# Kernel optimization log

Hardware: AMD Instinct MI355X
Metric: run time of the kernel (lower is better)

The kernel has to match this reference:

```python
import jax, jax.numpy as jnp
import numpy as np

B, S, L = 64, 512, 768


def setup_inputs() -> dict:
    key = jax.random.key(0)
    k1, k2 = jax.random.split(key)
    x = jax.random.normal(k1, (B, S, L), dtype=jnp.float32)
    # matches torch uniform_(-0.1, 0.1) init for the probe matrix b
    b = jax.random.uniform(k2, (L, L), minval=-0.1, maxval=0.1, dtype=jnp.float32)
    return {"x": x, "b": b}


def reference(x, b):
    # Original: z[b,i,j,h] = x_i - x_j; h = einsum('gh,bijh', b, z); dist = sum_g h^2
    # Identity: ||b @ (x_i - x_j)||^2 = ||p_i||^2 + ||p_j||^2 - 2 p_i . p_j,  p = x @ b^T
    p = jnp.einsum('gh,bsh->bsg', b, x)          # [B, S, L] projected points
    sq = jnp.sum(p * p, axis=-1)                 # [B, S]  squared norms
    gram = jnp.einsum('bsg,btg->bst', p, p)      # [B, S, S] inner products
    return sq[:, :, None] + sq[:, None, :] - 2.0 * gram  # [B, S, S]
```

## Files before the change

### kernel.cpp

```cpp
#include <hip/hip_runtime.h>
#include <hip/hip_bf16.h>


using bf16x8 = __attribute__((ext_vector_type(8))) __bf16;
using f32x4  = __attribute__((ext_vector_type(4))) float;
using fl4    = __attribute__((ext_vector_type(4))) float;
using u16x4  = __attribute__((ext_vector_type(4))) unsigned short;
using u32x4  = __attribute__((ext_vector_type(4))) unsigned int;

#define NB 64
#define NS 512
#define NL 768

__device__ __forceinline__ unsigned short f2bf(float f) {
  unsigned u = __builtin_bit_cast(unsigned, f);
  u += 0x7FFFu + ((u >> 16) & 1u);
  return (unsigned short)(u >> 16);
}

__device__ __forceinline__ void gload_lds16(const void* g, void* l) {
  __builtin_amdgcn_global_load_lds(
      (const __attribute__((address_space(1))) void*)g,
      (__attribute__((address_space(3))) void*)l, 16, 0, 0);
}

__device__ __forceinline__ bf16x8 cvt_bf8(fl4 a, fl4 b) {
  unsigned r0, r1, r2, r3;
  asm("v_cvt_pk_bf16_f32 %0, %1, %2" : "=v"(r0) : "v"(a[0]), "v"(a[1]));
  asm("v_cvt_pk_bf16_f32 %0, %1, %2" : "=v"(r1) : "v"(a[2]), "v"(a[3]));
  asm("v_cvt_pk_bf16_f32 %0, %1, %2" : "=v"(r2) : "v"(b[0]), "v"(b[1]));
  asm("v_cvt_pk_bf16_f32 %0, %1, %2" : "=v"(r3) : "v"(b[2]), "v"(b[3]));
  u32x4 t = {r0, r1, r2, r3};
  return __builtin_bit_cast(bf16x8, t);
}

__global__ __launch_bounds__(256) void k_cvt_b(const float* __restrict__ b,
                                               unsigned short* __restrict__ bb) {
  const long t = (long)blockIdx.x * 256 + threadIdx.x;
  fl4 v = *(const fl4*)(b + t * 4);
  u16x4 o;
#pragma unroll
  for (int j = 0; j < 4; ++j) o[j] = f2bf(v[j]);
  *(u16x4*)(bb + t * 4) = o;
}

__global__ __launch_bounds__(256) void k_proj(const float* __restrict__ x,
                                              const unsigned short* __restrict__ bb,
                                              unsigned short* __restrict__ p) {
  __shared__ __align__(16) float          smA[2][128 * 32];
  __shared__ __align__(16) unsigned short smB[2][128 * 32];
  const int tid = threadIdx.x;
  const int w = tid >> 6, l = tid & 63;
  const int wg = ((blockIdx.x & 7) * 192) + (blockIdx.x >> 3);
  const int nt = wg % 6, mt = wg / 6;
  const long m0 = (long)mt * 128, n0 = (long)nt * 128;
  const int wr = (w >> 1) * 64, wc = (w & 1) * 64;

  const int arow = tid >> 3;
  const int acol = ((tid & 7) ^ (arow & 7)) * 4;
  const float* gA = x + (m0 + arow) * (long)NL + acol;
  const int brow = tid >> 2;
  const int bcol = ((tid & 3) ^ (brow & 3)) * 8;
  const unsigned short* gB = bb + (n0 + brow) * (long)NL + bcol;

  const int qh = l >> 4, lr = l & 15;
  const int aoff = (wr + lr) * 128;
  const int asw1 = (qh * 32) ^ ((lr & 7) << 4);
  const int asw2 = (qh * 32 + 16) ^ ((lr & 7) << 4);
  const int boff = (wc + lr) * 64 + ((qh ^ (lr & 3)) << 4);

  f32x4 acc[4][4] = {};

#define STAGE_A(k0, buf)                                                     \
  {                                                                          \
    char* d_ = (char*)&smA[buf][0] + w * 1024;                               \
    const float* s_ = gA + (k0);                                             \
    gload_lds16(s_ + 0 * 32 * NL, d_ + 0 * 4096);                            \
    gload_lds16(s_ + 1 * 32 * NL, d_ + 1 * 4096);                            \
    gload_lds16(s_ + 2 * 32 * NL, d_ + 2 * 4096);                            \
    gload_lds16(s_ + 3 * 32 * NL, d_ + 3 * 4096);                            \
  }
#define STAGE_B(k0, buf)                                                     \
  {                                                                          \
    char* d_ = (char*)&smB[buf][0] + w * 1024;                               \
    const unsigned short* s_ = gB + (k0);                                    \
    gload_lds16(s_, d_);                                                     \
    gload_lds16(s_ + 64 * NL, d_ + 4096);                                    \
  }

  STAGE_A(0, 0)
  STAGE_B(0, 0)
  __syncthreads();
  int cur = 0;
#pragma unroll 1
  for (int kt = 0; kt < 24; ++kt) {
    if (kt < 23) {
      STAGE_A((kt + 1) * 32, cur ^ 1)
      STAGE_B((kt + 1) * 32, cur ^ 1)
    }
    const char* A  = (const char*)&smA[cur][0];
    const char* Bb = (const char*)&smB[cur][0];
    bf16x8 fa[4], fb[4];
#pragma unroll
    for (int m = 0; m < 4; ++m) {
      fl4 a0 = *(const fl4*)(A + aoff + m * 2048 + asw1);
      fl4 a1 = *(const fl4*)(A + aoff + m * 2048 + asw2);
      fa[m] = cvt_bf8(a0, a1);
    }
#pragma unroll
    for (int n = 0; n < 4; ++n)
      fb[n] = *(const bf16x8*)(Bb + boff + n * 1024);
#pragma unroll
    for (int m = 0; m < 4; ++m)
#pragma unroll
      for (int n = 0; n < 4; ++n)
        acc[m][n] = __builtin_amdgcn_mfma_f32_16x16x32_bf16(fa[m], fb[n], acc[m][n], 0, 0, 0);
    __syncthreads();
    cur ^= 1;
  }
#undef STAGE_A
#undef STAGE_B
#pragma unroll
  for (int m = 0; m < 4; ++m) {
    const long rbase = m0 + wr + m * 16 + qh * 4;
#pragma unroll
    for (int n = 0; n < 4; ++n) {
      const long col = n0 + wc + n * 16 + lr;
#pragma unroll
      for (int r = 0; r < 4; ++r)
        p[(rbase + r) * NL + col] = f2bf(acc[m][n][r]);
    }
  }
}

__global__ __launch_bounds__(256) void k_sq(const unsigned short* __restrict__ p,
                                            float* __restrict__ sq) {
  const int row = blockIdx.x * 4 + (threadIdx.x >> 6);
  const int l = threadIdx.x & 63;
  const unsigned short* pr = p + (long)row * NL;
  float s = 0.f;
#pragma unroll
  for (int c = 0; c < 3; ++c) {
    u16x4 v = *(const u16x4*)(pr + (c * 64 + l) * 4);
#pragma unroll
    for (int j = 0; j < 4; ++j) {
      float f = __builtin_bit_cast(float, ((unsigned)v[j]) << 16);
      s += f * f;
    }
  }
#pragma unroll
  for (int d = 32; d >= 1; d >>= 1) s += __shfl_xor(s, d, 64);
  if (l == 0) sq[row] = s;
}

__global__ __launch_bounds__(256) void k_gram(const unsigned short* __restrict__ p,
                                              const float* __restrict__ sq,
                                              float* __restrict__ out) {
  __shared__ __align__(16) unsigned short smA[2][128 * 32];
  __shared__ __align__(16) unsigned short smB[2][128 * 32];
  const int tid = threadIdx.x;
  const int w = tid >> 6, l = tid & 63;
  const int wg = ((blockIdx.x & 7) * 128) + (blockIdx.x >> 3);
  const int batch = wg >> 4, tile = wg & 15;
  const int mt = tile >> 2, nt = tile & 3;
  const unsigned short* pb = p + (long)batch * NS * NL;
  const long m0 = (long)mt * 128, n0 = (long)nt * 128;
  const int wr = (w >> 1) * 64, wc = (w & 1) * 64;

  const int srow = tid >> 2;
  const int scol = ((tid & 3) ^ (srow & 3)) * 8;
  const unsigned short* gA = pb + (m0 + srow) * (long)NL + scol;
  const unsigned short* gB = pb + (n0 + srow) * (long)NL + scol;

  const int qh = l >> 4, lr = l & 15;
  const int aoff = (wr + lr) * 64 + ((qh ^ (lr & 3)) << 4);
  const int boff = (wc + lr) * 64 + ((qh ^ (lr & 3)) << 4);

  f32x4 acc[4][4] = {};

#define STAGE2(k0, buf)                                                      \
  {                                                                          \
    char* da_ = (char*)&smA[buf][0] + w * 1024;                              \
    char* db_ = (char*)&smB[buf][0] + w * 1024;                              \
    gload_lds16(gA + (k0), da_);                                             \
    gload_lds16(gA + (k0) + 64 * NL, da_ + 4096);                            \
    gload_lds16(gB + (k0), db_);                                             \
    gload_lds16(gB + (k0) + 64 * NL, db_ + 4096);                            \
  }

  STAGE2(0, 0)
  __syncthreads();
  int cur = 0;
#pragma unroll 1
  for (int kt = 0; kt < 24; ++kt) {
    if (kt < 23) STAGE2((kt + 1) * 32, cur ^ 1)
    const char* A  = (const char*)&smA[cur][0];
    const char* Bb = (const char*)&smB[cur][0];
    bf16x8 fa[4], fb[4];
#pragma unroll
    for (int m = 0; m < 4; ++m)
      fa[m] = *(const bf16x8*)(A + aoff + m * 1024);
#pragma unroll
    for (int n = 0; n < 4; ++n)
      fb[n] = *(const bf16x8*)(Bb + boff + n * 1024);
#pragma unroll
    for (int m = 0; m < 4; ++m)
#pragma unroll
      for (int n = 0; n < 4; ++n)
        acc[m][n] = __builtin_amdgcn_mfma_f32_16x16x32_bf16(fa[m], fb[n], acc[m][n], 0, 0, 0);
    __syncthreads();
    cur ^= 1;
  }
#undef STAGE2
  const float* sqb = sq + batch * NS;
  float* outb = out + (long)batch * NS * NS;
  float sqc[4];
#pragma unroll
  for (int n = 0; n < 4; ++n) sqc[n] = sqb[n0 + wc + n * 16 + lr];
#pragma unroll
  for (int m = 0; m < 4; ++m) {
#pragma unroll
    for (int r = 0; r < 4; ++r) {
      const long row = m0 + wr + m * 16 + qh * 4 + r;
      const float sr = sqb[row];
#pragma unroll
      for (int n = 0; n < 4; ++n) {
        const long col = n0 + wc + n * 16 + lr;
        outb[row * NS + col] = sr + sqc[n] - 2.0f * acc[m][n][r];
      }
    }
  }
}

extern "C" void kernel_launch(void* const* d_in, const int* in_sizes, int n_in,
                              void* d_out, int out_size, void* d_ws, size_t ws_size,
                              hipStream_t stream) {
  (void)in_sizes; (void)n_in; (void)out_size; (void)ws_size;
  const float* x = (const float*)d_in[0];
  const float* b = (const float*)d_in[1];
  float* out = (float*)d_out;
  char* ws = (char*)d_ws;
  unsigned short* bb = (unsigned short*)ws;
  float* sq          = (float*)(ws + 1179648);
  unsigned short* p  = (unsigned short*)(ws + 1310720);

  k_cvt_b<<<576, 256, 0, stream>>>(b, bb);
  k_proj <<<1536, 256, 0, stream>>>(x, bb, p);
  k_sq   <<<8192, 256, 0, stream>>>(p, sq);
  k_gram <<<1024, 256, 0, stream>>>(p, sq, out);
}
```

Measured before the change: 118.7 us.

## Triple-buffer LDS staging with prefetch distance two in projection and gram GEMMs

```diff
diff --git a/kernel.cpp b/kernel.cpp
--- a/kernel.cpp
+++ b/kernel.cpp
@@ -34,6 +34,8 @@
   return __builtin_bit_cast(bf16x8, t);
 }
 
+#define MEMFENCE asm volatile("" ::: "memory")
+
 __global__ __launch_bounds__(256) void k_cvt_b(const float* __restrict__ b,
                                                unsigned short* __restrict__ bb) {
   const long t = (long)blockIdx.x * 256 + threadIdx.x;
@@ -47,8 +49,8 @@
 __global__ __launch_bounds__(256) void k_proj(const float* __restrict__ x,
                                               const unsigned short* __restrict__ bb,
                                               unsigned short* __restrict__ p) {
-  __shared__ __align__(16) float          smA[2][128 * 32];
-  __shared__ __align__(16) unsigned short smB[2][128 * 32];
+  __shared__ __align__(16) float          smA[3][128 * 32];
+  __shared__ __align__(16) unsigned short smB[3][128 * 32];
   const int tid = threadIdx.x;
   const int w = tid >> 6, l = tid & 63;
   const int wg = ((blockIdx.x & 7) * 192) + (blockIdx.x >> 3);
@@ -87,39 +89,52 @@
     gload_lds16(s_, d_);                                                     \
     gload_lds16(s_ + 64 * NL, d_ + 4096);                                    \
   }
-
-  STAGE_A(0, 0)
-  STAGE_B(0, 0)
-  __syncthreads();
-  int cur = 0;
+#define COMPUTE(buf)                                                         \
+  {                                                                          \
+    const char* A_  = (const char*)&smA[buf][0];                             \
+    const char* B_  = (const char*)&smB[buf][0];                             \
+    bf16x8 fa[4], fb[4];                                                     \
+    _Pragma("unroll")                                                        \
+    for (int m = 0; m < 4; ++m) {                                            \
+      fl4 a0 = *(const fl4*)(A_ + aoff + m * 2048 + asw1);                   \
+      fl4 a1 = *(const fl4*)(A_ + aoff + m * 2048 + asw2);                   \
+      fa[m] = cvt_bf8(a0, a1);                                               \
+    }                                                                        \
+    _Pragma("unroll")                                                        \
+    for (int n = 0; n < 4; ++n)                                              \
+      fb[n] = *(const bf16x8*)(B_ + boff + n * 1024);                        \
+    _Pragma("unroll")                                                        \
+    for (int m = 0; m < 4; ++m)                                              \
+      _Pragma("unroll")                                                      \
+      for (int n = 0; n < 4; ++n)                                            \
+        acc[m][n] = __builtin_amdgcn_mfma_f32_16x16x32_bf16(fa[m], fb[n],    \
+                                                            acc[m][n], 0, 0, 0); \
+  }
+
+  STAGE_A(0, 0)  STAGE_B(0, 0)
+  STAGE_A(32, 1) STAGE_B(32, 1)
+  int cur = 0, nxt2 = 2;
 #pragma unroll 1
-  for (int kt = 0; kt < 24; ++kt) {
-    if (kt < 23) {
-      STAGE_A((kt + 1) * 32, cur ^ 1)
-      STAGE_B((kt + 1) * 32, cur ^ 1)
-    }
-    const char* A  = (const char*)&smA[cur][0];
-    const char* Bb = (const char*)&smB[cur][0];
-    bf16x8 fa[4], fb[4];
-#pragma unroll
-    for (int m = 0; m < 4; ++m) {
-      fl4 a0 = *(const fl4*)(A + aoff + m * 2048 + asw1);
-      fl4 a1 = *(const fl4*)(A + aoff + m * 2048 + asw2);
-      fa[m] = cvt_bf8(a0, a1);
-    }
-#pragma unroll
-    for (int n = 0; n < 4; ++n)
-      fb[n] = *(const bf16x8*)(Bb + boff + n * 1024);
-#pragma unroll
-    for (int m = 0; m < 4; ++m)
-#pragma unroll
-      for (int n = 0; n < 4; ++n)
-        acc[m][n] = __builtin_amdgcn_mfma_f32_16x16x32_bf16(fa[m], fb[n], acc[m][n], 0, 0, 0);
-    __syncthreads();
-    cur ^= 1;
-  }
+  for (int kt = 0; kt < 23; ++kt) {
+    asm volatile("s_waitcnt vmcnt(6)" ::: "memory");
+    __builtin_amdgcn_s_barrier();
+    MEMFENCE;
+    if (kt < 22) {
+      STAGE_A((kt + 2) * 32, nxt2)
+      STAGE_B((kt + 2) * 32, nxt2)
+    }
+    COMPUTE(cur)
+    cur = (cur == 2) ? 0 : cur + 1;
+    nxt2 = (nxt2 == 2) ? 0 : nxt2 + 1;
+  }
+  asm volatile("s_waitcnt vmcnt(0)" ::: "memory");
+  __builtin_amdgcn_s_barrier();
+  MEMFENCE;
+  COMPUTE(cur)
 #undef STAGE_A
 #undef STAGE_B
+#undef COMPUTE
+
 #pragma unroll
   for (int m = 0; m < 4; ++m) {
     const long rbase = m0 + wr + m * 16 + qh * 4;
@@ -156,8 +171,8 @@
 __global__ __launch_bounds__(256) void k_gram(const unsigned short* __restrict__ p,
                                               const float* __restrict__ sq,
                                               float* __restrict__ out) {
-  __shared__ __align__(16) unsigned short smA[2][128 * 32];
-  __shared__ __align__(16) unsigned short smB[2][128 * 32];
+  __shared__ __align__(16) unsigned short smA[3][128 * 32];
+  __shared__ __align__(16) unsigned short smB[3][128 * 32];
   const int tid = threadIdx.x;
   const int w = tid >> 6, l = tid & 63;
   const int wg = ((blockIdx.x & 7) * 128) + (blockIdx.x >> 3);
@@ -187,31 +202,45 @@
     gload_lds16(gB + (k0), db_);                                             \
     gload_lds16(gB + (k0) + 64 * NL, db_ + 4096);                            \
   }
+#define COMPUTE2(buf)                                                        \
+  {                                                                          \
+    const char* A_ = (const char*)&smA[buf][0];                              \
+    const char* B_ = (const char*)&smB[buf][0];                              \
+    bf16x8 fa[4], fb[4];                                                     \
+    _Pragma("unroll")                                                        \
+    for (int m = 0; m < 4; ++m)                                              \
+      fa[m] = *(const bf16x8*)(A_ + aoff + m * 1024);                        \
+    _Pragma("unroll")                                                        \
+    for (int n = 0; n < 4; ++n)                                              \
+      fb[n] = *(const bf16x8*)(B_ + boff + n * 1024);                        \
+    _Pragma("unroll")                                                        \
+    for (int m = 0; m < 4; ++m)                                              \
+      _Pragma("unroll")                                                      \
+      for (int n = 0; n < 4; ++n)                                            \
+        acc[m][n] = __builtin_amdgcn_mfma_f32_16x16x32_bf16(fa[m], fb[n],    \
+                                                            acc[m][n], 0, 0, 0); \
+  }
 
   STAGE2(0, 0)
-  __syncthreads();
-  int cur = 0;
+  STAGE2(32, 1)
+  int cur = 0, nxt2 = 2;
 #pragma unroll 1
-  for (int kt = 0; kt < 24; ++kt) {
-    if (kt < 23) STAGE2((kt + 1) * 32, cur ^ 1)
-    const char* A  = (const char*)&smA[cur][0];
-    const char* Bb = (const char*)&smB[cur][0];
-    bf16x8 fa[4], fb[4];
-#pragma unroll
-    for (int m = 0; m < 4; ++m)
-      fa[m] = *(const bf16x8*)(A + aoff + m * 1024);
-#pragma unroll
-    for (int n = 0; n < 4; ++n)
-      fb[n] = *(const bf16x8*)(Bb + boff + n * 1024);
-#pragma unroll
-    for (int m = 0; m < 4; ++m)
-#pragma unroll
-      for (int n = 0; n < 4; ++n)
-        acc[m][n] = __builtin_amdgcn_mfma_f32_16x16x32_bf16(fa[m], fb[n], acc[m][n], 0, 0, 0);
-    __syncthreads();
-    cur ^= 1;
-  }
+  for (int kt = 0; kt < 23; ++kt) {
+    asm volatile("s_waitcnt vmcnt(4)" ::: "memory");
+    __builtin_amdgcn_s_barrier();
+    MEMFENCE;
+    if (kt < 22) STAGE2((kt + 2) * 32, nxt2)
+    COMPUTE2(cur)
+    cur = (cur == 2) ? 0 : cur + 1;
+    nxt2 = (nxt2 == 2) ? 0 : nxt2 + 1;
+  }
+  asm volatile("s_waitcnt vmcnt(0)" ::: "memory");
+  __builtin_amdgcn_s_barrier();
+  MEMFENCE;
+  COMPUTE2(cur)
 #undef STAGE2
+#undef COMPUTE2
+
   const float* sqb = sq + batch * NS;
   float* outb = out + (long)batch * NS * NS;
   float sqc[4];
```

After: 131.8 us. 1.11x slower.
